# Optimization experiments

Measured on AMD Instinct MI355X. Metric: run time of the kernel, lower is better.

Reference implementation:

```python
import jax, jax.numpy as jnp
import numpy as np

N = 100000
E = 1600000
IN_CH = 64
EDGE_DIM = 32
OUT_CH = 64
HEADS = 4
HEAD_CH = OUT_CH // HEADS
NEG_SLOPE = 0.2


def setup_inputs() -> dict:
    key = jax.random.key(0)
    k1, k2, k3, k4, k5 = jax.random.split(key, 5)
    x = jax.random.normal(k1, (N, IN_CH), dtype=jnp.float32)
    edge_index = jax.random.randint(k2, (2, E), 0, N, dtype=jnp.int64)
    edge_feature = jax.random.normal(k3, (E, EDGE_DIM), dtype=jnp.float32)
    # linear_msg: Linear(in_channels + edge_dim, out_channels, bias=False); torch weight is [out, in]
    W_msg = jax.random.normal(k4, (OUT_CH, IN_CH + EDGE_DIM), dtype=jnp.float32) * (1.0 / np.sqrt(IN_CH + EDGE_DIM))
    # att_msg: [1, heads, head_channels], glorot init
    att_msg = jax.random.normal(k5, (1, HEADS, HEAD_CH), dtype=jnp.float32) * np.sqrt(2.0 / (HEADS + HEAD_CH))
    return {"x": x, "edge_index": edge_index, "edge_feature": edge_feature, "W_msg": W_msg, "att_msg": att_msg}


def reference(x, edge_index, edge_feature, W_msg, att_msg):
    src = edge_index[0]  # x_j (source, gathered for messages)
    dst = edge_index[1]  # x_i / edge_index_i (softmax + aggregation groups)
    # per-edge gather + concat + linear (no bias)
    msg = jnp.concatenate([x[src], edge_feature], axis=-1) @ W_msg.T  # [E, OUT_CH]
    msg = msg.reshape(-1, HEADS, HEAD_CH)  # [E, H, Dh]
    # attention logits per head
    alpha = jnp.sum(msg * att_msg, axis=-1)  # [E, H]
    alpha = jnp.where(alpha >= 0, alpha, NEG_SLOPE * alpha)  # leaky_relu
    # segment softmax over destination nodes (PyG softmax: subtract max, / (sum + 1e-16))
    seg_max = jax.ops.segment_max(alpha, dst, num_segments=N)  # [N, H]
    alpha = jnp.exp(alpha - seg_max[dst])
    seg_sum = jax.ops.segment_sum(alpha, dst, num_segments=N)  # [N, H]
    alpha = alpha / (seg_sum[dst] + 1e-16)
    # weighted scatter-add aggregation (aggr='add', norm is None)
    out = jax.ops.segment_sum(msg * alpha[..., None], dst, num_segments=N)  # [N, H, Dh]
    return out.reshape(N, OUT_CH)
```

## Files before the change

### kernel.cpp

```cpp
#include <hip/hip_runtime.h>
#include <cstdint>
#include <cstddef>

constexpr int NN   = 100000;
constexpr int NE   = 1600000;
constexpr int CIN  = 64;
constexpr int CE   = 32;
constexpr int CCAT = 96;
constexpr int COUT = 64;
constexpr int NH   = 4;

constexpr int SCAN_B = 512;
constexpr int NBLK   = (NN + SCAN_B - 1) / SCAN_B;

__global__ void k_watt(const float* __restrict__ W, const float* __restrict__ att,
                       float* __restrict__ watt) {
  int t = blockIdx.x * blockDim.x + threadIdx.x;
  if (t < NH * CCAT) {
    int h = t / CCAT, k = t - h * CCAT;
    float s = 0.f;
#pragma unroll
    for (int d = 0; d < 16; ++d)
      s += att[h * 16 + d] * W[(h * 16 + d) * CCAT + k];
    watt[t] = s;
  }
}

__global__ __launch_bounds__(256) void k_xw(const float* __restrict__ x,
                                            const float* __restrict__ W,
                                            const float* __restrict__ watt,
                                            float* __restrict__ xw,
                                            float* __restrict__ xa) {
  int n = blockIdx.x * 256 + threadIdx.x;
  if (n >= NN) return;
  float xi[CIN];
  const float4* xp = reinterpret_cast<const float4*>(x + (size_t)n * CIN);
#pragma unroll
  for (int j = 0; j < CIN / 4; ++j) {
    float4 v = xp[j];
    xi[4 * j + 0] = v.x; xi[4 * j + 1] = v.y;
    xi[4 * j + 2] = v.z; xi[4 * j + 3] = v.w;
  }
  float4* xwp = reinterpret_cast<float4*>(xw + (size_t)n * COUT);
  for (int d0 = 0; d0 < COUT; d0 += 4) {
    float a0 = 0.f, a1 = 0.f, a2 = 0.f, a3 = 0.f;
#pragma unroll
    for (int k = 0; k < CIN; ++k) {
      float xv = xi[k];
      a0 += xv * W[(d0 + 0) * CCAT + k];
      a1 += xv * W[(d0 + 1) * CCAT + k];
      a2 += xv * W[(d0 + 2) * CCAT + k];
      a3 += xv * W[(d0 + 3) * CCAT + k];
    }
    xwp[d0 >> 2] = make_float4(a0, a1, a2, a3);
  }
#pragma unroll
  for (int h = 0; h < NH; ++h) {
    float a = 0.f;
#pragma unroll
    for (int k = 0; k < CIN; ++k) a += xi[k] * watt[h * CCAT + k];
    xa[n * NH + h] = a;
  }
}

__global__ __launch_bounds__(256) void k_hist(const int* __restrict__ ei,
                                              int* __restrict__ deg) {
  int e = blockIdx.x * 256 + threadIdx.x;
  if (e < NE) atomicAdd(&deg[ei[NE + e]], 1);
}

__global__ __launch_bounds__(SCAN_B) void k_scan1(const int* __restrict__ deg,
                                                  int* __restrict__ iscan,
                                                  int* __restrict__ bsum) {
  __shared__ int lds[SCAN_B];
  int t = threadIdx.x, i = blockIdx.x * SCAN_B + t;
  int v = (i < NN) ? deg[i] : 0;
  lds[t] = v;
  __syncthreads();
  for (int off = 1; off < SCAN_B; off <<= 1) {
    int u = (t >= off) ? lds[t - off] : 0;
    __syncthreads();
    lds[t] += u;
    __syncthreads();
  }
  if (i < NN) iscan[i] = lds[t];
  if (t == SCAN_B - 1) bsum[blockIdx.x] = lds[t];
}

__global__ __launch_bounds__(256) void k_scan2(const int* __restrict__ bsum,
                                               int* __restrict__ boff) {
  __shared__ int lds[256];
  int t = threadIdx.x;
  int v = (t < NBLK) ? bsum[t] : 0;
  lds[t] = v;
  __syncthreads();
  for (int off = 1; off < 256; off <<= 1) {
    int u = (t >= off) ? lds[t - off] : 0;
    __syncthreads();
    lds[t] += u;
    __syncthreads();
  }
  if (t < NBLK) boff[t] = lds[t] - v;
}

__global__ __launch_bounds__(256) void k_scan3(const int* __restrict__ iscan,
                                               const int* __restrict__ deg,
                                               const int* __restrict__ boff,
                                               int* __restrict__ start,
                                               int* __restrict__ cursor) {
  int i = blockIdx.x * 256 + threadIdx.x;
  if (i < NN) {
    int s = iscan[i] - deg[i] + boff[i / SCAN_B];
    start[i] = s;
    cursor[i] = s;
  }
  if (i == 0) start[NN] = NE;
}

__global__ __launch_bounds__(256) void k_edge(const int* __restrict__ ei,
                                              const float* __restrict__ ef,
                                              const float* __restrict__ watt,
                                              const float* __restrict__ xa,
                                              int* __restrict__ cursor,
                                              int2* __restrict__ es,
                                              float* __restrict__ lg) {
  int e = blockIdx.x * 256 + threadIdx.x;
  if (e >= NE) return;
  int src = ei[e];
  int dst = ei[NE + e];

  float f[CE];
  const float4* fp = reinterpret_cast<const float4*>(ef + (size_t)e * CE);
#pragma unroll
  for (int j = 0; j < CE / 4; ++j) {
    float4 v = fp[j];
    f[4 * j + 0] = v.x; f[4 * j + 1] = v.y;
    f[4 * j + 2] = v.z; f[4 * j + 3] = v.w;
  }
  float4 xav = *reinterpret_cast<const float4*>(xa + (size_t)src * NH);
  float a[NH] = {xav.x, xav.y, xav.z, xav.w};
#pragma unroll
  for (int h = 0; h < NH; ++h) {
    float acc = a[h];
#pragma unroll
    for (int k = 0; k < CE; ++k)
      acc += f[k] * watt[h * CCAT + CIN + k];
    a[h] = (acc >= 0.f) ? acc : 0.2f * acc;
  }

  int slot = atomicAdd(&cursor[dst], 1);
  es[slot] = make_int2(e, src);
  *reinterpret_cast<float4*>(lg + (size_t)slot * NH) =
      make_float4(a[0], a[1], a[2], a[3]);
}

__global__ __launch_bounds__(256) void k_norm(const int* __restrict__ start,
                                              float* __restrict__ lg,
                                              float* __restrict__ rs) {
  int n = blockIdx.x * 256 + threadIdx.x;
  if (n >= NN) return;
  int s0 = start[n], s1 = start[n + 1];
  float4 m = make_float4(-INFINITY, -INFINITY, -INFINITY, -INFINITY);
  float4* lg4 = reinterpret_cast<float4*>(lg);
  for (int s = s0; s < s1; ++s) {
    float4 v = lg4[s];
    m.x = fmaxf(m.x, v.x); m.y = fmaxf(m.y, v.y);
    m.z = fmaxf(m.z, v.z); m.w = fmaxf(m.w, v.w);
  }
  float4 sum = make_float4(0.f, 0.f, 0.f, 0.f);
  for (int s = s0; s < s1; ++s) {
    float4 v = lg4[s];
    v.x = __expf(v.x - m.x); v.y = __expf(v.y - m.y);
    v.z = __expf(v.z - m.z); v.w = __expf(v.w - m.w);
    lg4[s] = v;
    sum.x += v.x; sum.y += v.y; sum.z += v.z; sum.w += v.w;
  }
  *reinterpret_cast<float4*>(rs + (size_t)n * NH) =
      make_float4(1.f / (sum.x + 1e-16f), 1.f / (sum.y + 1e-16f),
                  1.f / (sum.z + 1e-16f), 1.f / (sum.w + 1e-16f));
}

__global__ __launch_bounds__(256) void k_agg(const int* __restrict__ start,
                                             const int2* __restrict__ es,
                                             const float* __restrict__ p,
                                             const float* __restrict__ rs,
                                             const float* __restrict__ ef,
                                             const float* __restrict__ W,
                                             const float* __restrict__ xw,
                                             float* __restrict__ out) {
  int wid = blockIdx.x * 4 + (threadIdx.x >> 6);
  int lane = threadIdx.x & 63;
  int s0 = __builtin_amdgcn_readfirstlane(start[wid]);
  int s1 = __builtin_amdgcn_readfirstlane(start[wid + 1]);
  int h = lane >> 4;

  float Wr[CE];
  const float4* wrp = reinterpret_cast<const float4*>(W + (size_t)lane * CCAT + CIN);
#pragma unroll
  for (int j = 0; j < CE / 4; ++j) {
    float4 v = wrp[j];
    Wr[4 * j + 0] = v.x; Wr[4 * j + 1] = v.y;
    Wr[4 * j + 2] = v.z; Wr[4 * j + 3] = v.w;
  }

  float acc0 = 0.f, acc1 = 0.f;

#define PROC(SLOT, ACC)                                                        \
  {                                                                            \
    int2 e2 = es[(SLOT)];                                                      \
    float pw = p[(size_t)(SLOT) * NH + h];                                     \
    float msg = xw[(size_t)e2.y * COUT + lane];                                \
    const float4* efp = reinterpret_cast<const float4*>(ef + (size_t)e2.x * CE); \
    _Pragma("unroll")                                                          \
    for (int j = 0; j < CE / 4; ++j) {                                         \
      float4 v = efp[j];                                                       \
      msg += v.x * Wr[4 * j + 0] + v.y * Wr[4 * j + 1] +                       \
             v.z * Wr[4 * j + 2] + v.w * Wr[4 * j + 3];                        \
    }                                                                          \
    ACC += pw * msg;                                                           \
  }

  int s = s0;
  for (; s + 1 < s1; s += 2) {
    PROC(s, acc0)
    PROC(s + 1, acc1)
  }
  if (s < s1) PROC(s, acc0)
#undef PROC

  float r = rs[(size_t)wid * NH + h];
  out[(size_t)wid * COUT + lane] = (acc0 + acc1) * r;
}

extern "C" void kernel_launch(void* const* d_in, const int* in_sizes, int n_in,
                              void* d_out, int out_size, void* d_ws, size_t ws_size,
                              hipStream_t stream) {
  const float* x   = (const float*)d_in[0];
  const int*   ei  = (const int*)d_in[1];
  const float* ef  = (const float*)d_in[2];
  const float* W   = (const float*)d_in[3];
  const float* att = (const float*)d_in[4];
  float* out = (float*)d_out;

  char* ws = (char*)d_ws;
  float* xw     = (float*)(ws + 0);
  float* xa     = (float*)(ws + 25600000);
  float* watt   = (float*)(ws + 27200000);
  int*   start  = (int*)  (ws + 27202048);
  float* rs     = (float*)(ws + 27602176);
  int2*  es     = (int2*) (ws + 29202176);
  float* lg     = (float*)(ws + 42002176);
  int*   deg    = (int*)  (ws + 67602176);
  int*   iscan  = (int*)  (ws + 68002176);
  int*   cursor = (int*)  (ws + 68402176);
  int*   bsum   = (int*)  (ws + 68802176);
  int*   boff   = (int*)  (ws + 68803200);

  hipMemsetAsync(deg, 0, (size_t)NN * 4, stream);

  k_watt<<<1, 384, 0, stream>>>(W, att, watt);
  k_xw<<<(NN + 255) / 256, 256, 0, stream>>>(x, W, watt, xw, xa);
  k_hist<<<(NE + 255) / 256, 256, 0, stream>>>(ei, deg);
  k_scan1<<<NBLK, SCAN_B, 0, stream>>>(deg, iscan, bsum);
  k_scan2<<<1, 256, 0, stream>>>(bsum, boff);
  k_scan3<<<(NN + 255) / 256, 256, 0, stream>>>(iscan, deg, boff, start, cursor);
  k_edge<<<(NE + 255) / 256, 256, 0, stream>>>(ei, ef, watt, xa, cursor, es, lg);
  k_norm<<<(NN + 255) / 256, 256, 0, stream>>>(start, lg, rs);
  k_agg<<<NN / 4, 256, 0, stream>>>(start, es, lg, rs, ef, W, xw, out);
}
```

Baseline: 931.0 us.

## Switch aggregation to edge-balanced waves with per-segment atomic flushes

Aggregation now gives each wave a fixed 64-slot chunk of the dst-sorted edge list instead of one destination node. Each wave flushes its per-node partial sums with atomicAdd whenever the destination changes, which balances work across waves regardless of degree skew. Edge metadata and logits are packed into one 32-byte record, and normalization runs one thread per (node, head) and folds the reciprocal sum into the stored weights. The cost is an extra memset of the output, atomic traffic to it, a third pass over the logits in normalization, and larger records to read.

After: 874.6 us. 1.06x faster.

```diff
diff --git a/kernel.cpp b/kernel.cpp
--- a/kernel.cpp
+++ b/kernel.cpp
@@ -12,6 +12,8 @@
 
 constexpr int SCAN_B = 512;
 constexpr int NBLK   = (NN + SCAN_B - 1) / SCAN_B;
+
+constexpr int SLOTS_PER_WAVE = 64;
 
 __global__ void k_watt(const float* __restrict__ W, const float* __restrict__ att,
                        float* __restrict__ watt) {
@@ -122,8 +124,7 @@
                                               const float* __restrict__ watt,
                                               const float* __restrict__ xa,
                                               int* __restrict__ cursor,
-                                              int2* __restrict__ es,
-                                              float* __restrict__ lg) {
+                                              float* __restrict__ rec) {
   int e = blockIdx.x * 256 + threadIdx.x;
   if (e >= NE) return;
   int src = ei[e];
@@ -149,49 +150,43 @@
   }
 
   int slot = atomicAdd(&cursor[dst], 1);
-  es[slot] = make_int2(e, src);
-  *reinterpret_cast<float4*>(lg + (size_t)slot * NH) =
-      make_float4(a[0], a[1], a[2], a[3]);
+  float4* rp = reinterpret_cast<float4*>(rec + (size_t)slot * 8);
+  float4 meta;
+  meta.x = __int_as_float(e);
+  meta.y = __int_as_float(src);
+  meta.z = __int_as_float(dst);
+  meta.w = 0.f;
+  rp[0] = meta;
+  rp[1] = make_float4(a[0], a[1], a[2], a[3]);
 }
 
 __global__ __launch_bounds__(256) void k_norm(const int* __restrict__ start,
-                                              float* __restrict__ lg,
-                                              float* __restrict__ rs) {
-  int n = blockIdx.x * 256 + threadIdx.x;
+                                              float* __restrict__ rec) {
+  int t = blockIdx.x * 256 + threadIdx.x;
+  int n = t >> 2, h = t & 3;
   if (n >= NN) return;
   int s0 = start[n], s1 = start[n + 1];
-  float4 m = make_float4(-INFINITY, -INFINITY, -INFINITY, -INFINITY);
-  float4* lg4 = reinterpret_cast<float4*>(lg);
+  float m = -INFINITY;
+  for (int s = s0; s < s1; ++s)
+    m = fmaxf(m, rec[(size_t)s * 8 + 4 + h]);
+  float sum = 0.f;
   for (int s = s0; s < s1; ++s) {
-    float4 v = lg4[s];
-    m.x = fmaxf(m.x, v.x); m.y = fmaxf(m.y, v.y);
-    m.z = fmaxf(m.z, v.z); m.w = fmaxf(m.w, v.w);
-  }
-  float4 sum = make_float4(0.f, 0.f, 0.f, 0.f);
-  for (int s = s0; s < s1; ++s) {
-    float4 v = lg4[s];
-    v.x = __expf(v.x - m.x); v.y = __expf(v.y - m.y);
-    v.z = __expf(v.z - m.z); v.w = __expf(v.w - m.w);
-    lg4[s] = v;
-    sum.x += v.x; sum.y += v.y; sum.z += v.z; sum.w += v.w;
-  }
-  *reinterpret_cast<float4*>(rs + (size_t)n * NH) =
-      make_float4(1.f / (sum.x + 1e-16f), 1.f / (sum.y + 1e-16f),
-                  1.f / (sum.z + 1e-16f), 1.f / (sum.w + 1e-16f));
-}
-
-__global__ __launch_bounds__(256) void k_agg(const int* __restrict__ start,
-                                             const int2* __restrict__ es,
-                                             const float* __restrict__ p,
-                                             const float* __restrict__ rs,
+    float p = __expf(rec[(size_t)s * 8 + 4 + h] - m);
+    rec[(size_t)s * 8 + 4 + h] = p;
+    sum += p;
+  }
+  float rs = 1.f / (sum + 1e-16f);
+  for (int s = s0; s < s1; ++s)
+    rec[(size_t)s * 8 + 4 + h] *= rs;
+}
+
+__global__ __launch_bounds__(256) void k_agg(const float* __restrict__ rec,
                                              const float* __restrict__ ef,
                                              const float* __restrict__ W,
                                              const float* __restrict__ xw,
                                              float* __restrict__ out) {
-  int wid = blockIdx.x * 4 + (threadIdx.x >> 6);
+  int gw = blockIdx.x * 4 + (threadIdx.x >> 6);
   int lane = threadIdx.x & 63;
-  int s0 = __builtin_amdgcn_readfirstlane(start[wid]);
-  int s1 = __builtin_amdgcn_readfirstlane(start[wid + 1]);
   int h = lane >> 4;
 
   float Wr[CE];
@@ -203,33 +198,40 @@
     Wr[4 * j + 2] = v.z; Wr[4 * j + 3] = v.w;
   }
 
-  float acc0 = 0.f, acc1 = 0.f;
-
-#define PROC(SLOT, ACC)                                                        \
-  {                                                                            \
-    int2 e2 = es[(SLOT)];                                                      \
-    float pw = p[(size_t)(SLOT) * NH + h];                                     \
-    float msg = xw[(size_t)e2.y * COUT + lane];                                \
-    const float4* efp = reinterpret_cast<const float4*>(ef + (size_t)e2.x * CE); \
-    _Pragma("unroll")                                                          \
-    for (int j = 0; j < CE / 4; ++j) {                                         \
-      float4 v = efp[j];                                                       \
-      msg += v.x * Wr[4 * j + 0] + v.y * Wr[4 * j + 1] +                       \
-             v.z * Wr[4 * j + 2] + v.w * Wr[4 * j + 3];                        \
-    }                                                                          \
-    ACC += pw * msg;                                                           \
-  }
-
-  int s = s0;
-  for (; s + 1 < s1; s += 2) {
-    PROC(s, acc0)
-    PROC(s + 1, acc1)
-  }
-  if (s < s1) PROC(s, acc0)
-#undef PROC
-
-  float r = rs[(size_t)wid * NH + h];
-  out[(size_t)wid * COUT + lane] = (acc0 + acc1) * r;
+  const float4* rp = reinterpret_cast<const float4*>(rec);
+  size_t sbase = (size_t)gw * SLOTS_PER_WAVE;
+
+  float acc = 0.f;
+  int cur = -1;
+#pragma unroll 4
+  for (int i = 0; i < SLOTS_PER_WAVE; ++i) {
+    size_t s = sbase + i;
+    float4 meta = rp[2 * s];
+    float4 p4   = rp[2 * s + 1];
+    int e   = __builtin_amdgcn_readfirstlane(__float_as_int(meta.x));
+    int src = __builtin_amdgcn_readfirstlane(__float_as_int(meta.y));
+    int dst = __builtin_amdgcn_readfirstlane(__float_as_int(meta.z));
+
+    if (dst != cur) {
+      if (cur >= 0) atomicAdd(&out[(size_t)cur * COUT + lane], acc);
+      acc = 0.f;
+      cur = dst;
+    }
+
+    float pw = (h & 2) ? ((h & 1) ? p4.w : p4.z)
+                       : ((h & 1) ? p4.y : p4.x);
+
+    float msg = xw[(size_t)src * COUT + lane];
+    const float4* efp = reinterpret_cast<const float4*>(ef + (size_t)e * CE);
+#pragma unroll
+    for (int j = 0; j < CE / 4; ++j) {
+      float4 v = efp[j];
+      msg += v.x * Wr[4 * j + 0] + v.y * Wr[4 * j + 1] +
+             v.z * Wr[4 * j + 2] + v.w * Wr[4 * j + 3];
+    }
+    acc += pw * msg;
+  }
+  atomicAdd(&out[(size_t)cur * COUT + lane], acc);
 }
 
 extern "C" void kernel_launch(void* const* d_in, const int* in_sizes, int n_in,
@@ -247,16 +249,15 @@
   float* xa     = (float*)(ws + 25600000);
   float* watt   = (float*)(ws + 27200000);
   int*   start  = (int*)  (ws + 27202048);
-  float* rs     = (float*)(ws + 27602176);
-  int2*  es     = (int2*) (ws + 29202176);
-  float* lg     = (float*)(ws + 42002176);
-  int*   deg    = (int*)  (ws + 67602176);
-  int*   iscan  = (int*)  (ws + 68002176);
-  int*   cursor = (int*)  (ws + 68402176);
-  int*   bsum   = (int*)  (ws + 68802176);
-  int*   boff   = (int*)  (ws + 68803200);
+  float* rec    = (float*)(ws + 27602176);
+  int*   deg    = (int*)  (ws + 78802176);
+  int*   iscan  = (int*)  (ws + 79202176);
+  int*   cursor = (int*)  (ws + 79602176);
+  int*   bsum   = (int*)  (ws + 80002176);
+  int*   boff   = (int*)  (ws + 80003200);
 
   hipMemsetAsync(deg, 0, (size_t)NN * 4, stream);
+  hipMemsetAsync(out, 0, (size_t)NN * COUT * 4, stream);
 
   k_watt<<<1, 384, 0, stream>>>(W, att, watt);
   k_xw<<<(NN + 255) / 256, 256, 0, stream>>>(x, W, watt, xw, xa);
@@ -264,7 +265,7 @@
   k_scan1<<<NBLK, SCAN_B, 0, stream>>>(deg, iscan, bsum);
   k_scan2<<<1, 256, 0, stream>>>(bsum, boff);
   k_scan3<<<(NN + 255) / 256, 256, 0, stream>>>(iscan, deg, boff, start, cursor);
-  k_edge<<<(NE + 255) / 256, 256, 0, stream>>>(ei, ef, watt, xa, cursor, es, lg);
-  k_norm<<<(NN + 255) / 256, 256, 0, stream>>>(start, lg, rs);
-  k_agg<<<NN / 4, 256, 0, stream>>>(start, es, lg, rs, ef, W, xw, out);
-}
+  k_edge<<<(NE + 255) / 256, 256, 0, stream>>>(ei, ef, watt, xa, cursor, rec);
+  k_norm<<<(NN * NH + 255) / 256, 256, 0, stream>>>(start, rec);
+  k_agg<<<(NE / SLOTS_PER_WAVE) / 4, 256, 0, stream>>>(rec, ef, W, xw, out);
+}
```
